# Optimization experiments

Hardware: AMD Instinct MI355X
Metric: run time of the kernel (lower is better)

## Reference

```python
import math
import jax, jax.numpy as jnp
import numpy as np

E = 8        # num_experts
TOPK = 2     # moe_top_k
CF = 1.25    # capacity_factor
EPS = 1e-5   # LayerNorm eps
NEG = -1e30  # sentinel for masked routing keys


def setup_inputs() -> dict:
    key = jax.random.key(0)
    ks = jax.random.split(key, 8)
    B, S, H, F = 4, 2048, 1024, 4096
    hidden_states = jax.random.normal(ks[0], (B, S, H), jnp.float32)
    token_mask = jnp.ones((B, S), jnp.int32)
    # router: Linear(H -> E), weight init N(0, 0.001), zero bias
    Wr = jax.random.normal(ks[1], (H, E), jnp.float32) * 0.001
    br = jnp.zeros((E,), jnp.float32)
    # per-expert MLP weights stacked along expert axis
    W1 = jax.random.normal(ks[2], (E, H, F), jnp.float32) * (1.0 / np.sqrt(H))
    b1 = jax.random.normal(ks[3], (E, F), jnp.float32) * 0.01
    W2 = jax.random.normal(ks[4], (E, F, H), jnp.float32) * (1.0 / np.sqrt(F))
    b2 = jax.random.normal(ks[5], (E, H), jnp.float32) * 0.01
    gamma = jnp.ones((H,), jnp.float32)
    beta = jnp.zeros((H,), jnp.float32)
    return {"hidden_states": hidden_states, "Wr": Wr, "br": br, "W1": W1,
            "b1": b1, "W2": W2, "b2": b2, "gamma": gamma, "beta": beta,
            "token_mask": token_mask}


def _layer_norm(x, gamma, beta):
    mu = jnp.mean(x, axis=-1, keepdims=True)
    var = jnp.mean((x - mu) ** 2, axis=-1, keepdims=True)
    return (x - mu) * jax.lax.rsqrt(var + EPS) * gamma + beta


def reference(hidden_states, Wr, br, W1, b1, W2, b2, gamma, beta, token_mask):
    # route_mask_pad_tokens=False and jitter=0 -> token_mask ignored, no noise
    B, S, H = hidden_states.shape
    x = hidden_states.reshape(-1, H)              # [N, H]
    N = x.shape[0]
    logits = x @ Wr + br                          # [N, E]
    top_vals, top_idx = jax.lax.top_k(logits, TOPK)  # [N, K]
    w = jax.nn.softmax(top_vals, axis=-1)         # [N, K]

    flat_idx = top_idx.reshape(-1)                # [N*K] expert per assignment
    flat_tok = jnp.repeat(jnp.arange(N), TOPK)    # [N*K] token per assignment
    w_flat = w.reshape(-1)                        # [N*K]

    cap = max(int(math.ceil(N / E * CF)), 1)
    # per-expert keys: weight if assignment routed to e else NEG  -> [E, N*K]
    key_mat = jnp.where(flat_idx[None, :] == jnp.arange(E)[:, None],
                        w_flat[None, :], NEG)
    # keep top-cap assignments by gate weight per expert (capacity drop)
    kv, ki = jax.lax.top_k(key_mat, cap)          # [E, cap]
    valid = kv > NEG / 2                          # real assignments only
    tok = flat_tok[ki]                            # [E, cap] token ids
    gate = jnp.where(valid, w_flat[ki], 0.0)      # [E, cap]

    xe = x[tok]                                   # [E, cap, H] gather
    h1 = jnp.einsum('ech,ehf->ecf', xe, W1) + b1[:, None, :]
    h1 = jax.nn.gelu(h1, approximate=False)       # torch nn.GELU (erf)
    y = jnp.einsum('ecf,efh->ech', h1, W2) + b2[:, None, :]

    out = jnp.zeros_like(x).at[tok.reshape(-1)].add(
        (y * gate[..., None]).reshape(-1, H))     # scatter-add combine
    out = out.reshape(B, S, H) + hidden_states    # residual
    return _layer_norm(out, gamma, beta)
```

## Files before the change

kernel.cpp:

```cpp
#include <hip/hip_runtime.h>
#include <math.h>

#define N_TOK 8192
#define H_DIM 1024
#define E_NUM 8
#define F_DIM 4096
#define CAP   1280
#define NA    (N_TOK*2)

typedef short   short8  __attribute__((ext_vector_type(8)));
typedef float   floatx4 __attribute__((ext_vector_type(4)));

__device__ __forceinline__ unsigned short f2b(float f) {
  unsigned u = __float_as_uint(f);
  unsigned r = (u + 0x7fffu + ((u >> 16) & 1u)) >> 16;
  return (unsigned short)r;
}

__device__ __forceinline__ void async_cp16(const void* g, void* l) {
  __builtin_amdgcn_global_load_lds(
      (__attribute__((address_space(1))) void*)(void*)g,
      (__attribute__((address_space(3))) void*)l, 16, 0, 0);
}

__global__ __launch_bounds__(256) void transpose_cvt(const float* __restrict__ src,
                                                     unsigned short* __restrict__ dst,
                                                     int R, int C) {
  __shared__ float tile[32][33];
  const int e  = blockIdx.z;
  const int r0 = blockIdx.y * 32, c0 = blockIdx.x * 32;
  const int tx = threadIdx.x, ty = threadIdx.y;
  const float* s = src + (size_t)e * R * C;
  unsigned short* d = dst + (size_t)e * R * C;
#pragma unroll
  for (int i = 0; i < 32; i += 8)
    tile[ty + i][tx] = s[(size_t)(r0 + ty + i) * C + c0 + tx];
  __syncthreads();
#pragma unroll
  for (int i = 0; i < 32; i += 8)
    d[(size_t)(c0 + ty + i) * R + r0 + tx] = f2b(tile[tx][ty + i]);
}

__global__ __launch_bounds__(256) void router_kernel(const float* __restrict__ x,
                                                     const float* __restrict__ Wr,
                                                     const float* __restrict__ br,
                                                     int* __restrict__ eid,
                                                     float* __restrict__ wf) {
  const int token = blockIdx.x * 4 + (threadIdx.x >> 6);
  const int lane  = threadIdx.x & 63;
  const float* xr = x + (size_t)token * H_DIM;
  float acc[E_NUM];
#pragma unroll
  for (int e = 0; e < E_NUM; ++e) acc[e] = 0.f;
  for (int h = lane; h < H_DIM; h += 64) {
    const float xv = xr[h];
    const float* wr = Wr + h * E_NUM;
#pragma unroll
    for (int e = 0; e < E_NUM; ++e) acc[e] += xv * wr[e];
  }
#pragma unroll
  for (int off = 32; off > 0; off >>= 1) {
#pragma unroll
    for (int e = 0; e < E_NUM; ++e) acc[e] += __shfl_down(acc[e], off, 64);
  }
  if (lane == 0) {
#pragma unroll
    for (int e = 0; e < E_NUM; ++e) acc[e] += br[e];
    int i0 = 0;
#pragma unroll
    for (int e = 1; e < E_NUM; ++e) if (acc[e] > acc[i0]) i0 = e;
    int i1 = (i0 == 0) ? 1 : 0;
    for (int e = 0; e < E_NUM; ++e) if (e != i0 && acc[e] > acc[i1]) i1 = e;
    const float ex = expf(acc[i1] - acc[i0]);
    const float inv = 1.f / (1.f + ex);
    eid[token * 2]     = i0;
    eid[token * 2 + 1] = i1;
    wf[token * 2]      = inv;
    wf[token * 2 + 1]  = ex * inv;
  }
}

#define MAXEQ 4096
__global__ __launch_bounds__(256) void select_kernel(const int* __restrict__ eid,
                                                     const float* __restrict__ wf,
                                                     int* __restrict__ tok_e,
                                                     float* __restrict__ gate_e) {
  const int e = blockIdx.x;
  const int tid = threadIdx.x;
  __shared__ unsigned hist[256];
  __shared__ unsigned sPrefix, sNeed, sKeepAll, sSlot, eqCnt;
  __shared__ int eq[MAXEQ];
  if (tid == 0) { sPrefix = 0; sNeed = CAP; sKeepAll = 0; sSlot = 0; eqCnt = 0; }
  __syncthreads();
  for (int level = 0; level < 4; ++level) {
    hist[tid] = 0;
    __syncthreads();
    const unsigned pref = sPrefix;
    const int shift = 24 - level * 8;
    for (int i = tid; i < NA; i += 256) {
      if (eid[i] == e) {
        const unsigned wb = __float_as_uint(wf[i]);
        if (level == 0 || (wb >> (shift + 8)) == pref)
          atomicAdd(&hist[(wb >> shift) & 255u], 1u);
      }
    }
    __syncthreads();
    if (tid == 0) {
      const unsigned need = sNeed;
      if (level == 0) {
        unsigned tot = 0;
        for (int b = 0; b < 256; ++b) tot += hist[b];
        if (tot <= (unsigned)CAP) sKeepAll = 1;
      }
      if (!sKeepAll) {
        unsigned cum = 0; int b = 255;
        for (; b > 0; --b) {
          if (cum + hist[b] >= need) break;
          cum += hist[b];
        }
        sPrefix = (sPrefix << 8) | (unsigned)b;
        sNeed = need - cum;
      }
    }
    __syncthreads();
    if (sKeepAll) break;
  }
  const unsigned keepAll = sKeepAll;
  const unsigned thr = sPrefix;
  for (int i = tid; i < NA; i += 256) {
    if (eid[i] != e) continue;
    const unsigned wb = __float_as_uint(wf[i]);
    if (keepAll || wb > thr) {
      const unsigned s = atomicAdd(&sSlot, 1u);
      tok_e[e * CAP + s]  = i >> 1;
      gate_e[e * CAP + s] = wf[i];
    } else if (wb == thr) {
      const unsigned p = atomicAdd(&eqCnt, 1u);
      if (p < MAXEQ) eq[p] = i;
    }
  }
  __syncthreads();
  if (!keepAll) {
    const int r = (int)sNeed;
    const int t = min((int)eqCnt, MAXEQ);
    for (int a2 = tid; a2 < t; a2 += 256) {
      const int idx = eq[a2];
      int rank = 0;
      for (int b2 = 0; b2 < t; ++b2) rank += (eq[b2] < idx);
      if (rank < r) {
        const unsigned s = atomicAdd(&sSlot, 1u);
        tok_e[e * CAP + s]  = idx >> 1;
        gate_e[e * CAP + s] = wf[idx];
      }
    }
  }
}

__global__ __launch_bounds__(128) void gather_kernel(const float* __restrict__ x,
                                                     const int* __restrict__ tok_e,
                                                     unsigned short* __restrict__ xe) {
  const int s = blockIdx.x;
  const int t = threadIdx.x;
  const int tok = tok_e[s];
  uint4* dst = (uint4*)(xe + (size_t)s * H_DIM) + t;
  if (tok < 0) { uint4 z; z.x = z.y = z.z = z.w = 0u; *dst = z; return; }
  const float4* xp = (const float4*)x + (size_t)tok * (H_DIM / 4);
  const float4 v0 = xp[t * 2], v1 = xp[t * 2 + 1];
  uint4 u;
  u.x = (unsigned)f2b(v0.x) | ((unsigned)f2b(v0.y) << 16);
  u.y = (unsigned)f2b(v0.z) | ((unsigned)f2b(v0.w) << 16);
  u.z = (unsigned)f2b(v1.x) | ((unsigned)f2b(v1.y) << 16);
  u.w = (unsigned)f2b(v1.z) | ((unsigned)f2b(v1.w) << 16);
  *dst = u;
}

__device__ __forceinline__ void mfma_loop(const unsigned short* Ab,
                                          const unsigned short* Bb,
                                          int Kdim, floatx4 acc[4][4],
                                          unsigned short* As, unsigned short* Bs) {
  const int tid  = threadIdx.x;
  const int lane = tid & 63;
  const int w    = tid >> 6;
  const int wm   = (w >> 1) * 64, wn = (w & 1) * 64;
  const int lrow = lane & 15, lk = (lane >> 4) * 8;
  const int r0 = tid >> 2;
  const int c0 = (tid & 3) * 8;
  const int r1 = (tid + 256) >> 2;
  for (int k0 = 0; k0 < Kdim; k0 += 32) {
    async_cp16(Ab + (size_t)r0 * Kdim + k0 + c0, As + tid * 8);
    async_cp16(Ab + (size_t)r1 * Kdim + k0 + c0, As + (tid + 256) * 8);
    async_cp16(Bb + (size_t)r0 * Kdim + k0 + c0, Bs + tid * 8);
    async_cp16(Bb + (size_t)r1 * Kdim + k0 + c0, Bs + (tid + 256) * 8);
    __syncthreads();
    short8 a[4], b[4];
#pragma unroll
    for (int i = 0; i < 4; ++i)
      a[i] = *(const short8*)(As + (wm + i * 16 + lrow) * 32 + lk);
#pragma unroll
    for (int i = 0; i < 4; ++i)
      b[i] = *(const short8*)(Bs + (wn + i * 16 + lrow) * 32 + lk);
#pragma unroll
    for (int mi = 0; mi < 4; ++mi)
#pragma unroll
      for (int ni = 0; ni < 4; ++ni)
        acc[mi][ni] = __builtin_amdgcn_mfma_f32_16x16x32_bf16(a[mi], b[ni], acc[mi][ni], 0, 0, 0);
    __syncthreads();
  }
}

__global__ __launch_bounds__(256) void gemm1_kernel(const unsigned short* __restrict__ xe,
                                                    const unsigned short* __restrict__ WT,
                                                    const float* __restrict__ b1,
                                                    unsigned short* __restrict__ h1) {
  __shared__ unsigned short As[128 * 32], Bs[128 * 32];
  const int e  = blockIdx.z;
  const int m0 = blockIdx.y * 128, n0 = blockIdx.x * 128;
  const unsigned short* Ab = xe + ((size_t)e * CAP + m0) * H_DIM;
  const unsigned short* Bb = WT + ((size_t)e * F_DIM + n0) * H_DIM;
  floatx4 acc[4][4];
#pragma unroll
  for (int mi = 0; mi < 4; ++mi)
#pragma unroll
    for (int ni = 0; ni < 4; ++ni) acc[mi][ni] = (floatx4){0.f, 0.f, 0.f, 0.f};
  mfma_loop(Ab, Bb, H_DIM, acc, As, Bs);
  const int lane = threadIdx.x & 63, w = threadIdx.x >> 6;
  const int wm = (w >> 1) * 64, wn = (w & 1) * 64;
  const int col0  = n0 + wn + (lane & 15);
  const int rbase = m0 + wm + ((lane >> 4) * 4);
#pragma unroll
  for (int ni = 0; ni < 4; ++ni) {
    const int col = col0 + ni * 16;
    const float bias = b1[e * F_DIM + col];
#pragma unroll
    for (int mi = 0; mi < 4; ++mi) {
#pragma unroll
      for (int j = 0; j < 4; ++j) {
        const int row = rbase + mi * 16 + j;
        float v = acc[mi][ni][j] + bias;
        v = 0.5f * v * (1.0f + erff(v * 0.70710678118654752f));
        h1[((size_t)e * CAP + row) * F_DIM + col] = f2b(v);
      }
    }
  }
}

__global__ __launch_bounds__(256) void gemm2_kernel(const unsigned short* __restrict__ h1,
                                                    const unsigned short* __restrict__ WT,
                                                    const float* __restrict__ b2,
                                                    const int* __restrict__ tok_e,
                                                    const float* __restrict__ gate_e,
                                                    float* __restrict__ out) {
  __shared__ unsigned short As[128 * 32], Bs[128 * 32];
  const int e  = blockIdx.z;
  const int m0 = blockIdx.y * 128, n0 = blockIdx.x * 128;
  const unsigned short* Ab = h1 + ((size_t)e * CAP + m0) * F_DIM;
  const unsigned short* Bb = WT + ((size_t)e * H_DIM + n0) * F_DIM;
  floatx4 acc[4][4];
#pragma unroll
  for (int mi = 0; mi < 4; ++mi)
#pragma unroll
    for (int ni = 0; ni < 4; ++ni) acc[mi][ni] = (floatx4){0.f, 0.f, 0.f, 0.f};
  mfma_loop(Ab, Bb, F_DIM, acc, As, Bs);
  const int lane = threadIdx.x & 63, w = threadIdx.x >> 6;
  const int wm = (w >> 1) * 64, wn = (w & 1) * 64;
  const int col0  = n0 + wn + (lane & 15);
  const int rbase = m0 + wm + ((lane >> 4) * 4);
  float b2v[4];
#pragma unroll
  for (int ni = 0; ni < 4; ++ni) b2v[ni] = b2[e * H_DIM + col0 + ni * 16];
#pragma unroll
  for (int mi = 0; mi < 4; ++mi) {
#pragma unroll
    for (int j = 0; j < 4; ++j) {
      const int row = rbase + mi * 16 + j;
      const int tok = tok_e[e * CAP + row];
      if (tok < 0) continue;
      const float g = gate_e[e * CAP + row];
      float* orow = out + (size_t)tok * H_DIM;
#pragma unroll
      for (int ni = 0; ni < 4; ++ni) {
        const float v = acc[mi][ni][j] + b2v[ni];
        atomicAdd(orow + col0 + ni * 16, g * v);
      }
    }
  }
}

__global__ __launch_bounds__(256) void ln_kernel(float* __restrict__ out,
                                                 const float* __restrict__ gamma,
                                                 const float* __restrict__ beta) {
  const int token = blockIdx.x;
  const int tid = threadIdx.x;
  const int lane = tid & 63, w = tid >> 6;
  float* row = out + (size_t)token * H_DIM;
  float v[4];
#pragma unroll
  for (int i = 0; i < 4; ++i) v[i] = row[tid + i * 256];
  float s = v[0] + v[1] + v[2] + v[3];
  __shared__ float red[8];
#pragma unroll
  for (int off = 32; off > 0; off >>= 1) s += __shfl_down(s, off, 64);
  if (lane == 0) red[w] = s;
  __syncthreads();
  const float mu = (red[0] + red[1] + red[2] + red[3]) * (1.f / H_DIM);
  float q = 0.f;
#pragma unroll
  for (int i = 0; i < 4; ++i) { const float d = v[i] - mu; q += d * d; }
#pragma unroll
  for (int off = 32; off > 0; off >>= 1) q += __shfl_down(q, off, 64);
  if (lane == 0) red[4 + w] = q;
  __syncthreads();
  const float var = (red[4] + red[5] + red[6] + red[7]) * (1.f / H_DIM);
  const float rs = rsqrtf(var + 1e-5f);
#pragma unroll
  for (int i = 0; i < 4; ++i) {
    const int h = tid + i * 256;
    row[h] = (v[i] - mu) * rs * gamma[h] + beta[h];
  }
}

extern "C" void kernel_launch(void* const* d_in, const int* in_sizes, int n_in,
                              void* d_out, int out_size, void* d_ws, size_t ws_size,
                              hipStream_t stream) {
  const float* x     = (const float*)d_in[0];
  const float* Wr    = (const float*)d_in[1];
  const float* br    = (const float*)d_in[2];
  const float* W1    = (const float*)d_in[3];
  const float* b1    = (const float*)d_in[4];
  const float* W2    = (const float*)d_in[5];
  const float* b2    = (const float*)d_in[6];
  const float* gamma = (const float*)d_in[7];
  const float* beta  = (const float*)d_in[8];
  float* out = (float*)d_out;

  char* ws = (char*)d_ws;
  unsigned short* WT   = (unsigned short*)(ws);
  unsigned short* xe   = (unsigned short*)(ws + 67108864);
  unsigned short* h1   = (unsigned short*)(ws + 88080384);
  int*            eid  = (int*)(ws + 171966464);
  float*          wf   = (float*)(ws + 172032000);
  int*            tok_e  = (int*)(ws + 172097536);
  float*          gate_e = (float*)(ws + 172138496);

  transpose_cvt<<<dim3(F_DIM / 32, H_DIM / 32, E_NUM), dim3(32, 8), 0, stream>>>(W1, WT, H_DIM, F_DIM);
  router_kernel<<<N_TOK / 4, 256, 0, stream>>>(x, Wr, br, eid, wf);
  hipMemsetAsync(tok_e, 0xFF, E_NUM * CAP * sizeof(int), stream);
  hipMemsetAsync(gate_e, 0, E_NUM * CAP * sizeof(float), stream);
  select_kernel<<<E_NUM, 256, 0, stream>>>(eid, wf, tok_e, gate_e);
  gather_kernel<<<E_NUM * CAP, 128, 0, stream>>>(x, tok_e, xe);
  gemm1_kernel<<<dim3(F_DIM / 128, CAP / 128, E_NUM), 256, 0, stream>>>(xe, WT, b1, h1);
  transpose_cvt<<<dim3(H_DIM / 32, F_DIM / 32, E_NUM), dim3(32, 8), 0, stream>>>(W2, WT, F_DIM, H_DIM);
  hipMemcpyAsync(out, x, (size_t)N_TOK * H_DIM * sizeof(float), hipMemcpyDeviceToDevice, stream);
  gemm2_kernel<<<dim3(H_DIM / 128, CAP / 128, E_NUM), 256, 0, stream>>>(h1, WT, b2, tok_e, gate_e, out);
  ln_kernel<<<N_TOK, 256, 0, stream>>>(out, gamma, beta);
}
```

Before: 805.0 us.

## Vectorize weight transpose, widen select block, and split-K gemm2

The weight transpose-convert kernel now uses 64x64 tiles with float4 loads and 16-byte bf16 stores in place of scalar accesses. The expert capacity selection kernel runs 1024 threads per block instead of 256. gemm2 splits its K dimension in two across grid z, doubling the block count from 640 so more CUs stay busy, with the bias added only by the first split. The cost is twice as many atomic adds into the output.

```diff
diff --git a/kernel.cpp b/kernel.cpp
--- a/kernel.cpp
+++ b/kernel.cpp
@@ -7,6 +7,7 @@
 #define F_DIM 4096
 #define CAP   1280
 #define NA    (N_TOK*2)
+#define KSPLIT 2
 
 typedef short   short8  __attribute__((ext_vector_type(8)));
 typedef float   floatx4 __attribute__((ext_vector_type(4)));
@@ -26,19 +27,32 @@
 __global__ __launch_bounds__(256) void transpose_cvt(const float* __restrict__ src,
                                                      unsigned short* __restrict__ dst,
                                                      int R, int C) {
-  __shared__ float tile[32][33];
+  __shared__ float tile[64 * 68];
   const int e  = blockIdx.z;
-  const int r0 = blockIdx.y * 32, c0 = blockIdx.x * 32;
-  const int tx = threadIdx.x, ty = threadIdx.y;
+  const int r0 = blockIdx.y * 64, c0 = blockIdx.x * 64;
+  const int tid = threadIdx.x;
   const float* s = src + (size_t)e * R * C;
   unsigned short* d = dst + (size_t)e * R * C;
-#pragma unroll
-  for (int i = 0; i < 32; i += 8)
-    tile[ty + i][tx] = s[(size_t)(r0 + ty + i) * C + c0 + tx];
-  __syncthreads();
-#pragma unroll
-  for (int i = 0; i < 32; i += 8)
-    d[(size_t)(c0 + ty + i) * R + r0 + tx] = f2b(tile[tx][ty + i]);
+  const int rr = tid >> 4;
+  const int c4 = (tid & 15) * 4;
+#pragma unroll
+  for (int it = 0; it < 4; ++it) {
+    const int r = rr + it * 16;
+    const float4 v = *(const float4*)(s + (size_t)(r0 + r) * C + c0 + c4);
+    *(float4*)(&tile[r * 68 + c4]) = v;
+  }
+  __syncthreads();
+  const int cc = tid >> 3;
+  const int r8 = (tid & 7) * 8;
+#pragma unroll
+  for (int it = 0; it < 2; ++it) {
+    const int c = cc + it * 32;
+    uint4 u;
+    unsigned short* pu = (unsigned short*)&u;
+#pragma unroll
+    for (int i = 0; i < 8; ++i) pu[i] = f2b(tile[(r8 + i) * 68 + c]);
+    *(uint4*)(d + (size_t)(c0 + c) * R + r0 + r8) = u;
+  }
 }
 
 __global__ __launch_bounds__(256) void router_kernel(const float* __restrict__ x,
@@ -81,10 +95,10 @@
 }
 
 #define MAXEQ 4096
-__global__ __launch_bounds__(256) void select_kernel(const int* __restrict__ eid,
-                                                     const float* __restrict__ wf,
-                                                     int* __restrict__ tok_e,
-                                                     float* __restrict__ gate_e) {
+__global__ __launch_bounds__(1024) void select_kernel(const int* __restrict__ eid,
+                                                      const float* __restrict__ wf,
+                                                      int* __restrict__ tok_e,
+                                                      float* __restrict__ gate_e) {
   const int e = blockIdx.x;
   const int tid = threadIdx.x;
   __shared__ unsigned hist[256];
@@ -93,11 +107,11 @@
   if (tid == 0) { sPrefix = 0; sNeed = CAP; sKeepAll = 0; sSlot = 0; eqCnt = 0; }
   __syncthreads();
   for (int level = 0; level < 4; ++level) {
-    hist[tid] = 0;
+    if (tid < 256) hist[tid] = 0;
     __syncthreads();
     const unsigned pref = sPrefix;
     const int shift = 24 - level * 8;
-    for (int i = tid; i < NA; i += 256) {
+    for (int i = tid; i < NA; i += 1024) {
       if (eid[i] == e) {
         const unsigned wb = __float_as_uint(wf[i]);
         if (level == 0 || (wb >> (shift + 8)) == pref)
@@ -127,7 +141,7 @@
   }
   const unsigned keepAll = sKeepAll;
   const unsigned thr = sPrefix;
-  for (int i = tid; i < NA; i += 256) {
+  for (int i = tid; i < NA; i += 1024) {
     if (eid[i] != e) continue;
     const unsigned wb = __float_as_uint(wf[i]);
     if (keepAll || wb > thr) {
@@ -143,7 +157,7 @@
   if (!keepAll) {
     const int r = (int)sNeed;
     const int t = min((int)eqCnt, MAXEQ);
-    for (int a2 = tid; a2 < t; a2 += 256) {
+    for (int a2 = tid; a2 < t; a2 += 1024) {
       const int idx = eq[a2];
       int rank = 0;
       for (int b2 = 0; b2 < t; ++b2) rank += (eq[b2] < idx);
@@ -176,7 +190,8 @@
 
 __device__ __forceinline__ void mfma_loop(const unsigned short* Ab,
                                           const unsigned short* Bb,
-                                          int Kdim, floatx4 acc[4][4],
+                                          int kBeg, int kEnd, int ld,
+                                          floatx4 acc[4][4],
                                           unsigned short* As, unsigned short* Bs) {
   const int tid  = threadIdx.x;
   const int lane = tid & 63;
@@ -186,11 +201,11 @@
   const int r0 = tid >> 2;
   const int c0 = (tid & 3) * 8;
   const int r1 = (tid + 256) >> 2;
-  for (int k0 = 0; k0 < Kdim; k0 += 32) {
-    async_cp16(Ab + (size_t)r0 * Kdim + k0 + c0, As + tid * 8);
-    async_cp16(Ab + (size_t)r1 * Kdim + k0 + c0, As + (tid + 256) * 8);
-    async_cp16(Bb + (size_t)r0 * Kdim + k0 + c0, Bs + tid * 8);
-    async_cp16(Bb + (size_t)r1 * Kdim + k0 + c0, Bs + (tid + 256) * 8);
+  for (int k0 = kBeg; k0 < kEnd; k0 += 32) {
+    async_cp16(Ab + (size_t)r0 * ld + k0 + c0, As + tid * 8);
+    async_cp16(Ab + (size_t)r1 * ld + k0 + c0, As + (tid + 256) * 8);
+    async_cp16(Bb + (size_t)r0 * ld + k0 + c0, Bs + tid * 8);
+    async_cp16(Bb + (size_t)r1 * ld + k0 + c0, Bs + (tid + 256) * 8);
     __syncthreads();
     short8 a[4], b[4];
 #pragma unroll
@@ -222,7 +237,7 @@
   for (int mi = 0; mi < 4; ++mi)
 #pragma unroll
     for (int ni = 0; ni < 4; ++ni) acc[mi][ni] = (floatx4){0.f, 0.f, 0.f, 0.f};
-  mfma_loop(Ab, Bb, H_DIM, acc, As, Bs);
+  mfma_loop(Ab, Bb, 0, H_DIM, H_DIM, acc, As, Bs);
   const int lane = threadIdx.x & 63, w = threadIdx.x >> 6;
   const int wm = (w >> 1) * 64, wn = (w & 1) * 64;
   const int col0  = n0 + wn + (lane & 15);
@@ -251,7 +266,9 @@
                                                     const float* __restrict__ gate_e,
                                                     float* __restrict__ out) {
   __shared__ unsigned short As[128 * 32], Bs[128 * 32];
-  const int e  = blockIdx.z;
+  const int z  = blockIdx.z;
+  const int e  = z >> 1;
+  const int kc = z & 1;
   const int m0 = blockIdx.y * 128, n0 = blockIdx.x * 128;
   const unsigned short* Ab = h1 + ((size_t)e * CAP + m0) * F_DIM;
   const unsigned short* Bb = WT + ((size_t)e * H_DIM + n0) * F_DIM;
@@ -260,14 +277,16 @@
   for (int mi = 0; mi < 4; ++mi)
 #pragma unroll
     for (int ni = 0; ni < 4; ++ni) acc[mi][ni] = (floatx4){0.f, 0.f, 0.f, 0.f};
-  mfma_loop(Ab, Bb, F_DIM, acc, As, Bs);
+  const int kLen = F_DIM / KSPLIT;
+  mfma_loop(Ab, Bb, kc * kLen, kc * kLen + kLen, F_DIM, acc, As, Bs);
   const int lane = threadIdx.x & 63, w = threadIdx.x >> 6;
   const int wm = (w >> 1) * 64, wn = (w & 1) * 64;
   const int col0  = n0 + wn + (lane & 15);
   const int rbase = m0 + wm + ((lane >> 4) * 4);
   float b2v[4];
 #pragma unroll
-  for (int ni = 0; ni < 4; ++ni) b2v[ni] = b2[e * H_DIM + col0 + ni * 16];
+  for (int ni = 0; ni < 4; ++ni)
+    b2v[ni] = (kc == 0) ? b2[e * H_DIM + col0 + ni * 16] : 0.f;
 #pragma unroll
   for (int mi = 0; mi < 4; ++mi) {
 #pragma unroll
@@ -342,15 +361,15 @@
   int*            tok_e  = (int*)(ws + 172097536);
   float*          gate_e = (float*)(ws + 172138496);
 
-  transpose_cvt<<<dim3(F_DIM / 32, H_DIM / 32, E_NUM), dim3(32, 8), 0, stream>>>(W1, WT, H_DIM, F_DIM);
+  transpose_cvt<<<dim3(F_DIM / 64, H_DIM / 64, E_NUM), 256, 0, stream>>>(W1, WT, H_DIM, F_DIM);
   router_kernel<<<N_TOK / 4, 256, 0, stream>>>(x, Wr, br, eid, wf);
   hipMemsetAsync(tok_e, 0xFF, E_NUM * CAP * sizeof(int), stream);
   hipMemsetAsync(gate_e, 0, E_NUM * CAP * sizeof(float), stream);
-  select_kernel<<<E_NUM, 256, 0, stream>>>(eid, wf, tok_e, gate_e);
+  select_kernel<<<E_NUM, 1024, 0, stream>>>(eid, wf, tok_e, gate_e);
   gather_kernel<<<E_NUM * CAP, 128, 0, stream>>>(x, tok_e, xe);
   gemm1_kernel<<<dim3(F_DIM / 128, CAP / 128, E_NUM), 256, 0, stream>>>(xe, WT, b1, h1);
-  transpose_cvt<<<dim3(H_DIM / 32, F_DIM / 32, E_NUM), dim3(32, 8), 0, stream>>>(W2, WT, F_DIM, H_DIM);
+  transpose_cvt<<<dim3(H_DIM / 64, F_DIM / 64, E_NUM), 256, 0, stream>>>(W2, WT, F_DIM, H_DIM);
   hipMemcpyAsync(out, x, (size_t)N_TOK * H_DIM * sizeof(float), hipMemcpyDeviceToDevice, stream);
-  gemm2_kernel<<<dim3(H_DIM / 128, CAP / 128, E_NUM), 256, 0, stream>>>(h1, WT, b2, tok_e, gate_e, out);
+  gemm2_kernel<<<dim3(H_DIM / 128, CAP / 128, E_NUM * KSPLIT), 256, 0, stream>>>(h1, WT, b2, tok_e, gate_e, out);
   ln_kernel<<<N_TOK, 256, 0, stream>>>(out, gamma, beta);
 }
```

New measurement: 756.1 us. 6.1% less time.
